# Performance work log

Measured on AMD Instinct MI355X. Metric: run time of the kernel, lower is better.

Reference implementation:

```python
import jax, jax.numpy as jnp
import numpy as np

N = 100000
E = 1600000
BN_EPS = 1e-3  # Keras BatchNormalization default epsilon


def setup_inputs() -> dict:
    key = jax.random.key(0)
    ks = jax.random.split(key, 24)
    inp = {
        'x': jax.random.normal(ks[0], (N, 128), jnp.float32),
        'edge_src': jax.random.randint(ks[1], (E,), 0, N, jnp.int32),
        'edge_dst': jnp.sort(jax.random.randint(ks[2], (E,), 0, N, jnp.int32)),
        'edge_w': jax.random.uniform(ks[3], (E,), jnp.float32),
        'bn1_gamma': jnp.ones((128,), jnp.float32),
        'bn1_beta': jnp.zeros((128,), jnp.float32),
        'bn1_mean': jax.random.normal(ks[4], (128,), jnp.float32),
        'bn1_var': jax.random.uniform(ks[5], (128,), jnp.float32),
        'gat_w': jax.random.normal(ks[6], (128, 128), jnp.float32) * 0.09,
        'gat_a_self': jax.random.normal(ks[7], (128,), jnp.float32) * 0.09,
        'gat_a_nbr': jax.random.normal(ks[8], (128,), jnp.float32) * 0.09,
        'gat_b': jnp.zeros((128,), jnp.float32),
        'bn2_gamma': jnp.ones((128,), jnp.float32),
        'bn2_beta': jnp.zeros((128,), jnp.float32),
        'bn2_mean': jax.random.normal(ks[9], (128,), jnp.float32),
        'bn2_var': jax.random.uniform(ks[10], (128,), jnp.float32),
        'gcn2_w': jax.random.normal(ks[11], (128, 64), jnp.float32) * 0.09,
        'gcn2_b': jnp.zeros((64,), jnp.float32),
        'bn3_gamma': jnp.ones((64,), jnp.float32),
        'bn3_beta': jnp.zeros((64,), jnp.float32),
        'bn3_mean': jax.random.normal(ks[12], (64,), jnp.float32),
        'bn3_var': jax.random.uniform(ks[13], (64,), jnp.float32),
        'gcn3_w': jax.random.normal(ks[14], (64, 32), jnp.float32) * 0.12,
        'gcn3_b': jnp.zeros((32,), jnp.float32),
        'zm_w': jax.random.normal(ks[15], (32, 64), jnp.float32) * 0.18,
        'zm_b': jnp.zeros((64,), jnp.float32),
        'zv_w': jax.random.normal(ks[16], (32, 64), jnp.float32) * 0.18,
        'zv_b': jnp.zeros((64,), jnp.float32),
        'eps': jax.random.normal(ks[17], (N, 64), jnp.float32),
    }
    return inp


def _bn(x, gamma, beta, mean, var):
    # Keras BatchNormalization, inference mode (moving statistics).
    return gamma * (x - mean) * jax.lax.rsqrt(var + BN_EPS) + beta


def _gat(x, edge_src, edge_dst, w, a_self, a_nbr, b, n):
    h = x @ w                                   # [N, C]
    att_i = h @ a_self                          # [N] target score
    att_j = h @ a_nbr                           # [N] source score
    e = jax.nn.leaky_relu(att_i[edge_dst] + att_j[edge_src], 0.2)  # [E]
    m = jax.ops.segment_max(e, edge_dst, num_segments=n)
    p = jnp.exp(e - m[edge_dst])
    s = jax.ops.segment_sum(p, edge_dst, num_segments=n)
    alpha = p / s[edge_dst]                     # segment softmax over in-edges
    out = jax.ops.segment_sum(alpha[:, None] * h[edge_src], edge_dst, num_segments=n)
    return jax.nn.relu(out + b)


def _gcn(x, edge_src, edge_dst, edge_w, w, b, n):
    h = x @ w                                   # [N, C]
    out = jax.ops.segment_sum(edge_w[:, None] * h[edge_src], edge_dst, num_segments=n)
    return jax.nn.relu(out + b)


def reference(x, edge_src, edge_dst, edge_w,
              bn1_gamma, bn1_beta, bn1_mean, bn1_var,
              gat_w, gat_a_self, gat_a_nbr, gat_b,
              bn2_gamma, bn2_beta, bn2_mean, bn2_var,
              gcn2_w, gcn2_b,
              bn3_gamma, bn3_beta, bn3_mean, bn3_var,
              gcn3_w, gcn3_b,
              zm_w, zm_b, zv_w, zv_b, eps):
    n = x.shape[0]
    h = _bn(x, bn1_gamma, bn1_beta, bn1_mean, bn1_var)
    h = _gat(h, edge_src, edge_dst, gat_w, gat_a_self, gat_a_nbr, gat_b, n)
    # dropout layers are identity at inference
    h = _bn(h, bn2_gamma, bn2_beta, bn2_mean, bn2_var)
    h = _gcn(h, edge_src, edge_dst, edge_w, gcn2_w, gcn2_b, n)
    h = _bn(h, bn3_gamma, bn3_beta, bn3_mean, bn3_var)
    h = _gcn(h, edge_src, edge_dst, edge_w, gcn3_w, gcn3_b, n)
    # Flatten on [N, F] is identity
    z_mean = jax.nn.sigmoid(h @ zm_w + zm_b)
    z_log_var = h @ zv_w + zv_b
    z = z_mean + jnp.exp(0.5 * z_log_var) * eps
    return (z_mean, z_log_var, z)
```

## Files before the change

kernel.cpp:

```cpp
#include <hip/hip_runtime.h>
#include <math.h>


#define BN_EPS 1e-3f

__device__ __forceinline__ int swz(int i) { return i + ((i >> 5) << 2); }

__device__ __forceinline__ unsigned bf2(float lo, float hi) {
  unsigned ul = __float_as_uint(lo), uh = __float_as_uint(hi);
  ul = (ul + 0x7FFFu + ((ul >> 16) & 1u)) >> 16;
  uh = (uh + 0x7FFFu + ((uh >> 16) & 1u)) >> 16;
  return ul | (uh << 16);
}

__device__ __forceinline__ float4 ub4(uint2 p) {
  float4 r;
  r.x = __uint_as_float(p.x << 16);
  r.y = __uint_as_float(p.x & 0xFFFF0000u);
  r.z = __uint_as_float(p.y << 16);
  r.w = __uint_as_float(p.y & 0xFFFF0000u);
  return r;
}

__global__ __launch_bounds__(256) void prep_kernel(
    const float* __restrict__ bn1g, const float* __restrict__ bn1b,
    const float* __restrict__ bn1m, const float* __restrict__ bn1v,
    const float* __restrict__ gatw,
    const float* __restrict__ bn2g, const float* __restrict__ bn2b,
    const float* __restrict__ bn2m, const float* __restrict__ bn2v,
    const float* __restrict__ gcn2w,
    const float* __restrict__ bn3g, const float* __restrict__ bn3b,
    const float* __restrict__ bn3m, const float* __restrict__ bn3v,
    const float* __restrict__ gcn3w,
    float* __restrict__ W1f, float* __restrict__ bW1,
    float* __restrict__ W2f, float* __restrict__ bW2,
    float* __restrict__ W3f, float* __restrict__ bW3) {
  __shared__ float a1[128], b1[128], a2[128], b2[128], a3[64], b3[64];
  const int t = threadIdx.x;
  if (t < 128) {
    float a = bn1g[t] * (1.0f / sqrtf(bn1v[t] + BN_EPS));
    a1[t] = a; b1[t] = bn1b[t] - bn1m[t] * a;
    float c = bn2g[t] * (1.0f / sqrtf(bn2v[t] + BN_EPS));
    a2[t] = c; b2[t] = bn2b[t] - bn2m[t] * c;
    if (t < 64) {
      float d = bn3g[t] * (1.0f / sqrtf(bn3v[t] + BN_EPS));
      a3[t] = d; b3[t] = bn3b[t] - bn3m[t] * d;
    }
  }
  __syncthreads();
  for (int idx = t; idx < 128 * 128; idx += 256) W1f[idx] = a1[idx >> 7] * gatw[idx];
  for (int idx = t; idx < 128 * 64; idx += 256)  W2f[idx] = a2[idx >> 6] * gcn2w[idx];
  for (int idx = t; idx < 64 * 32; idx += 256)   W3f[idx] = a3[idx >> 5] * gcn3w[idx];
  if (t < 128) { float s = 0.f; for (int k = 0; k < 128; k++) s += b1[k] * gatw[k * 128 + t]; bW1[t] = s; }
  if (t < 64)  { float s = 0.f; for (int k = 0; k < 128; k++) s += b2[k] * gcn2w[k * 64 + t]; bW2[t] = s; }
  if (t < 32)  { float s = 0.f; for (int k = 0; k < 64; k++)  s += b3[k] * gcn3w[k * 32 + t]; bW3[t] = s; }
}

__global__ __launch_bounds__(256) void rowptr_kernel(
    const int* __restrict__ dst, int* __restrict__ rp, int n, int e) {
  int i = blockIdx.x * 256 + threadIdx.x;
  if (i > n) return;
  int lo = 0, hi = e;
  while (lo < hi) {
    int mid = (lo + hi) >> 1;
    if (dst[mid] < i) lo = mid + 1; else hi = mid;
  }
  rp[i] = lo;
}

template <int K, int C, int NN, int KC, bool DO_ATT>
__global__ __launch_bounds__(256) void gemm_tiled(
    const float* __restrict__ in, const float* __restrict__ Wf,
    const float* __restrict__ bW, unsigned short* __restrict__ outb, int n_nodes,
    const float* __restrict__ aself, const float* __restrict__ anbr,
    float* __restrict__ atti, float* __restrict__ attj) {
  constexpr int NCG = C / 8;
  constexpr int NNG = 256 / NCG;
  constexpr int NT = NNG * NN;
  constexpr int XROW = NT + (NT / 32) * 4;
  constexpr int WROW = C + (C / 32) * 4;
  constexpr int KCV = KC / 4;
  constexpr int CV = C / 4;
  static_assert(!DO_ATT || NCG == 16, "att fusion assumes 16 col-groups");
  __shared__ float xs[KC * XROW];
  __shared__ float wsm[KC * WROW];
  const int node0 = blockIdx.x * NT;
  const float4* __restrict__ x4 = (const float4*)in;
  const int cg = threadIdx.x % NCG;
  const int ng = threadIdx.x / NCG;
  const int xbase = swz(ng * NN);
  const int wbase = swz(cg * 8);
  float acc[NN][8] = {};
#pragma unroll
  for (int kc = 0; kc < K / KC; kc++) {
    if (kc) __syncthreads();
    for (int idx = threadIdx.x; idx < NT * KCV; idx += 256) {
      int row = idx / KCV, kg = idx % KCV;
      int gn = node0 + row;
      if (gn >= n_nodes) gn = n_nodes - 1;
      float4 v = x4[(size_t)gn * (K / 4) + kc * KCV + kg];
      int ns = swz(row);
      xs[(kg * 4 + 0) * XROW + ns] = v.x;
      xs[(kg * 4 + 1) * XROW + ns] = v.y;
      xs[(kg * 4 + 2) * XROW + ns] = v.z;
      xs[(kg * 4 + 3) * XROW + ns] = v.w;
    }
    for (int idx = threadIdx.x; idx < KC * CV; idx += 256) {
      int k = idx / CV, cv = idx % CV;
      float4 v = ((const float4*)Wf)[(size_t)(kc * KC + k) * CV + cv];
      *(float4*)&wsm[k * WROW + swz(cv * 4)] = v;
    }
    __syncthreads();
#pragma unroll 2
    for (int k = 0; k < KC; k++) {
      const float* xr = &xs[k * XROW + xbase];
      const float* wr = &wsm[k * WROW + wbase];
      float4 w0 = *(const float4*)wr;
      float4 w1 = *(const float4*)(wr + 4);
      float4 xa = *(const float4*)xr;
      float xv[NN];
      xv[0] = xa.x; xv[1] = xa.y; xv[2] = xa.z; xv[3] = xa.w;
      if (NN == 8) {
        float4 xb = *(const float4*)(xr + 4);
        xv[4] = xb.x; xv[5] = xb.y; xv[6] = xb.z; xv[7] = xb.w;
      }
#pragma unroll
      for (int i = 0; i < NN; i++) {
        acc[i][0] = fmaf(xv[i], w0.x, acc[i][0]);
        acc[i][1] = fmaf(xv[i], w0.y, acc[i][1]);
        acc[i][2] = fmaf(xv[i], w0.z, acc[i][2]);
        acc[i][3] = fmaf(xv[i], w0.w, acc[i][3]);
        acc[i][4] = fmaf(xv[i], w1.x, acc[i][4]);
        acc[i][5] = fmaf(xv[i], w1.y, acc[i][5]);
        acc[i][6] = fmaf(xv[i], w1.z, acc[i][6]);
        acc[i][7] = fmaf(xv[i], w1.w, acc[i][7]);
      }
    }
  }
  const int c0 = cg * 8;
  const float4 bv0 = *(const float4*)&bW[c0];
  const float4 bv1 = *(const float4*)&bW[c0 + 4];
  float si[NN], sj[NN];
  float4 as0, as1, an0, an1;
  if (DO_ATT) {
    as0 = *(const float4*)&aself[c0]; as1 = *(const float4*)&aself[c0 + 4];
    an0 = *(const float4*)&anbr[c0];  an1 = *(const float4*)&anbr[c0 + 4];
  }
#pragma unroll
  for (int i = 0; i < NN; i++) {
    float4 o0 = {acc[i][0] + bv0.x, acc[i][1] + bv0.y,
                 acc[i][2] + bv0.z, acc[i][3] + bv0.w};
    float4 o1 = {acc[i][4] + bv1.x, acc[i][5] + bv1.y,
                 acc[i][6] + bv1.z, acc[i][7] + bv1.w};
    int gn = node0 + ng * NN + i;
    if (gn < n_nodes) {
      uint4 pk;
      pk.x = bf2(o0.x, o0.y); pk.y = bf2(o0.z, o0.w);
      pk.z = bf2(o1.x, o1.y); pk.w = bf2(o1.z, o1.w);
      *(uint4*)&outb[(size_t)gn * C + c0] = pk;
    }
    if (DO_ATT) {
      si[i] = o0.x * as0.x + o0.y * as0.y + o0.z * as0.z + o0.w * as0.w +
              o1.x * as1.x + o1.y * as1.y + o1.z * as1.z + o1.w * as1.w;
      sj[i] = o0.x * an0.x + o0.y * an0.y + o0.z * an0.z + o0.w * an0.w +
              o1.x * an1.x + o1.y * an1.y + o1.z * an1.z + o1.w * an1.w;
    }
  }
  if (DO_ATT) {
#pragma unroll
    for (int off = 1; off < 16; off <<= 1) {
#pragma unroll
      for (int i = 0; i < NN; i++) {
        si[i] += __shfl_xor(si[i], off);
        sj[i] += __shfl_xor(sj[i], off);
      }
    }
    if (cg == 0) {
#pragma unroll
      for (int i = 0; i < NN; i++) {
        int gn = node0 + ng * NN + i;
        if (gn < n_nodes) { atti[gn] = si[i]; attj[gn] = sj[i]; }
      }
    }
  }
}

__global__ __launch_bounds__(256) void gat_kernel(
    const unsigned short* __restrict__ h1b, const float* __restrict__ att_i,
    const float* __restrict__ att_j, const int* __restrict__ src,
    const int* __restrict__ rp, const float* __restrict__ bias,
    float* __restrict__ out, int n) {
  const int node = (blockIdx.x * 256 + threadIdx.x) >> 6;
  const int lane = threadIdx.x & 63;
  if (node >= n) return;
  const int cg = lane & 31;
  const int eg = lane >> 5;
  const int start = rp[node];
  const int deg = rp[node + 1] - start;
  if (deg == 0) {
    if (eg == 0) {
      float4 b = ((const float4*)bias)[cg];
      float4 o = {fmaxf(b.x, 0.f), fmaxf(b.y, 0.f), fmaxf(b.z, 0.f), fmaxf(b.w, 0.f)};
      ((float4*)out)[(unsigned)node * 32 + cg] = o;
    }
    return;
  }
  const uint2* __restrict__ h2v = (const uint2*)h1b;
  const float ai = att_i[node];
  float4 av[4];
#pragma unroll
  for (int k = 0; k < 4; k++) av[k] = {0.f, 0.f, 0.f, 0.f};
  float ss = 0.f, m_run = -INFINITY;
  for (int chunk = 0; chunk < deg; chunk += 64) {
    const int cnt = min(64, deg - chunk);
    int sv = 0; float v = -INFINITY;
    if (lane < cnt) {
      sv = src[start + chunk + lane];
      float a = ai + att_j[sv];
      v = (a >= 0.f) ? a : 0.2f * a;
    }
    float m = v;
#pragma unroll
    for (int off = 32; off; off >>= 1) m = fmaxf(m, __shfl_xor(m, off));
    const float m_new = fmaxf(m_run, m);
    const float scale = expf(m_run - m_new);
#pragma unroll
    for (int k = 0; k < 4; k++) {
      av[k].x *= scale; av[k].y *= scale; av[k].z *= scale; av[k].w *= scale;
    }
    const float p = (lane < cnt) ? expf(v - m_new) : 0.f;
    float ps = p;
#pragma unroll
    for (int off = 32; off; off >>= 1) ps += __shfl_xor(ps, off);
    ss = ss * scale + ps;
    m_run = m_new;
    for (int j2 = 0; j2 < cnt; j2 += 16) {
      float pk[8]; int sk[8];
#pragma unroll
      for (int k = 0; k < 8; k++) {
        int j = j2 + 2 * k + eg;
        pk[k] = __shfl(p, j);
        sk[k] = __shfl(sv, j);
      }
      uint2 hk[8];
#pragma unroll
      for (int k = 0; k < 8; k++) hk[k] = h2v[(unsigned)sk[k] * 32 + cg];
#pragma unroll
      for (int k = 0; k < 8; k++) {
        float4 hv = ub4(hk[k]);
        av[k & 3].x = fmaf(pk[k], hv.x, av[k & 3].x);
        av[k & 3].y = fmaf(pk[k], hv.y, av[k & 3].y);
        av[k & 3].z = fmaf(pk[k], hv.z, av[k & 3].z);
        av[k & 3].w = fmaf(pk[k], hv.w, av[k & 3].w);
      }
    }
  }
  float4 a0;
  a0.x = av[0].x + av[1].x + av[2].x + av[3].x;
  a0.y = av[0].y + av[1].y + av[2].y + av[3].y;
  a0.z = av[0].z + av[1].z + av[2].z + av[3].z;
  a0.w = av[0].w + av[1].w + av[2].w + av[3].w;
  a0.x += __shfl_xor(a0.x, 32); a0.y += __shfl_xor(a0.y, 32);
  a0.z += __shfl_xor(a0.z, 32); a0.w += __shfl_xor(a0.w, 32);
  if (eg == 0) {
    const float inv = 1.0f / ss;
    float4 b = ((const float4*)bias)[cg];
    float4 o;
    o.x = fmaxf(fmaf(a0.x, inv, b.x), 0.f);
    o.y = fmaxf(fmaf(a0.y, inv, b.y), 0.f);
    o.z = fmaxf(fmaf(a0.z, inv, b.z), 0.f);
    o.w = fmaxf(fmaf(a0.w, inv, b.w), 0.f);
    ((float4*)out)[(unsigned)node * 32 + cg] = o;
  }
}

template <int C, int NCH>
__global__ __launch_bounds__(256) void gcn_agg_kernel(
    const unsigned short* __restrict__ hb, const int* __restrict__ src,
    const float* __restrict__ ew, const int* __restrict__ rp,
    const float* __restrict__ bias, float* __restrict__ out, int n) {
  constexpr int CG = C / 4;
  constexpr int EGN = 64 / CG;
  const int node = (blockIdx.x * 256 + threadIdx.x) >> 6;
  const int lane = threadIdx.x & 63;
  if (node >= n) return;
  const int cg = lane % CG;
  const int eg = lane / CG;
  const int start = rp[node];
  const int deg = rp[node + 1] - start;
  const uint2* __restrict__ h2v = (const uint2*)hb;
  float4 av[4];
#pragma unroll
  for (int k = 0; k < 4; k++) av[k] = {0.f, 0.f, 0.f, 0.f};
  for (int chunk = 0; chunk < deg; chunk += 64) {
    const int cnt = min(64, deg - chunk);
    int sv = 0; float wv = 0.f;
    if (lane < cnt) {
      sv = src[start + chunk + lane];
      wv = ew[start + chunk + lane];
    }
    for (int j2 = 0; j2 < cnt; j2 += NCH * EGN) {
      float wk[NCH]; int sk[NCH];
#pragma unroll
      for (int k = 0; k < NCH; k++) {
        int j = j2 + k * EGN + eg;
        wk[k] = __shfl(wv, j);
        sk[k] = __shfl(sv, j);
      }
      uint2 hk[NCH];
#pragma unroll
      for (int k = 0; k < NCH; k++) hk[k] = h2v[(unsigned)sk[k] * CG + cg];
#pragma unroll
      for (int k = 0; k < NCH; k++) {
        float4 hv = ub4(hk[k]);
        av[k & 3].x = fmaf(wk[k], hv.x, av[k & 3].x);
        av[k & 3].y = fmaf(wk[k], hv.y, av[k & 3].y);
        av[k & 3].z = fmaf(wk[k], hv.z, av[k & 3].z);
        av[k & 3].w = fmaf(wk[k], hv.w, av[k & 3].w);
      }
    }
  }
  float4 a0;
  a0.x = av[0].x + av[1].x + av[2].x + av[3].x;
  a0.y = av[0].y + av[1].y + av[2].y + av[3].y;
  a0.z = av[0].z + av[1].z + av[2].z + av[3].z;
  a0.w = av[0].w + av[1].w + av[2].w + av[3].w;
#pragma unroll
  for (int off = CG; off < 64; off <<= 1) {
    a0.x += __shfl_xor(a0.x, off); a0.y += __shfl_xor(a0.y, off);
    a0.z += __shfl_xor(a0.z, off); a0.w += __shfl_xor(a0.w, off);
  }
  if (eg == 0) {
    float4 b = ((const float4*)bias)[cg];
    float4 o;
    o.x = fmaxf(a0.x + b.x, 0.f); o.y = fmaxf(a0.y + b.y, 0.f);
    o.z = fmaxf(a0.z + b.z, 0.f); o.w = fmaxf(a0.w + b.w, 0.f);
    ((float4*)out)[(unsigned)node * CG + cg] = o;
  }
}

__global__ __launch_bounds__(256) void final_kernel(
    const float* __restrict__ g3, const float* __restrict__ zmw,
    const float* __restrict__ zmb, const float* __restrict__ zvw,
    const float* __restrict__ zvb, const float* __restrict__ eps,
    float* __restrict__ out, int n) {
  __shared__ float wm[32 * 64];
  __shared__ float wv[32 * 64];
  __shared__ float xs[4 * 32];
  for (int idx = threadIdx.x; idx < 2048; idx += 256) {
    wm[idx] = zmw[idx];
    wv[idx] = zvw[idx];
  }
  const float bm = zmb[threadIdx.x & 63];
  const float bv = zvb[threadIdx.x & 63];
  const size_t n64 = (size_t)n * 64;
  for (int pass = 0; pass < 16; pass++) {
    const int nb = blockIdx.x * 64 + pass * 4;
    __syncthreads();
    if (threadIdx.x < 128) {
      size_t idx = (size_t)nb * 32 + threadIdx.x;
      xs[threadIdx.x] = (idx < (size_t)n * 32) ? g3[idx] : 0.f;
    }
    __syncthreads();
    const int node = nb + (threadIdx.x >> 6);
    if (node >= n) continue;
    const int c = threadIdx.x & 63;
    const float* x = &xs[(threadIdx.x >> 6) * 32];
    float am = 0.f, avv = 0.f;
#pragma unroll
    for (int k = 0; k < 32; k++) {
      float xv = x[k];
      am = fmaf(xv, wm[k * 64 + c], am);
      avv = fmaf(xv, wv[k * 64 + c], avv);
    }
    am += bm;
    avv += bv;
    float zm = 1.f / (1.f + expf(-am));
    float ex = expf(fminf(0.5f * avv, 85.0f));
    float z = fmaf(ex, eps[(size_t)node * 64 + c], zm);
    size_t o = (size_t)node * 64 + c;
    out[o] = zm;
    out[n64 + o] = avv;
    out[2 * n64 + o] = z;
  }
}

extern "C" void kernel_launch(void* const* d_in, const int* in_sizes, int n_in,
                              void* d_out, int out_size, void* d_ws, size_t ws_size,
                              hipStream_t stream) {
  const float* x     = (const float*)d_in[0];
  const int*   esrc  = (const int*)d_in[1];
  const int*   edst  = (const int*)d_in[2];
  const float* ew    = (const float*)d_in[3];
  const float* bn1g  = (const float*)d_in[4];
  const float* bn1b  = (const float*)d_in[5];
  const float* bn1m  = (const float*)d_in[6];
  const float* bn1v  = (const float*)d_in[7];
  const float* gatw  = (const float*)d_in[8];
  const float* aself = (const float*)d_in[9];
  const float* anbr  = (const float*)d_in[10];
  const float* gatb  = (const float*)d_in[11];
  const float* bn2g  = (const float*)d_in[12];
  const float* bn2b  = (const float*)d_in[13];
  const float* bn2m  = (const float*)d_in[14];
  const float* bn2v  = (const float*)d_in[15];
  const float* gcn2w = (const float*)d_in[16];
  const float* gcn2b = (const float*)d_in[17];
  const float* bn3g  = (const float*)d_in[18];
  const float* bn3b  = (const float*)d_in[19];
  const float* bn3m  = (const float*)d_in[20];
  const float* bn3v  = (const float*)d_in[21];
  const float* gcn3w = (const float*)d_in[22];
  const float* gcn3b = (const float*)d_in[23];
  const float* zmw   = (const float*)d_in[24];
  const float* zmb   = (const float*)d_in[25];
  const float* zvw   = (const float*)d_in[26];
  const float* zvb   = (const float*)d_in[27];
  const float* eps   = (const float*)d_in[28];
  float* out = (float*)d_out;

  const int n = in_sizes[0] / 128;
  const int E = in_sizes[1];

  char* base = (char*)d_ws;
  size_t off = 0;
  auto alloc = [&](size_t bytes) -> char* {
    char* p = base + off;
    off += (bytes + 255) & ~(size_t)255;
    return p;
  };
  int*   rp   = (int*)alloc((size_t)(n + 1) * 4);
  float* W1f  = (float*)alloc(128 * 128 * 4);
  float* bW1  = (float*)alloc(128 * 4);
  float* W2f  = (float*)alloc(128 * 64 * 4);
  float* bW2  = (float*)alloc(64 * 4);
  float* W3f  = (float*)alloc(64 * 32 * 4);
  float* bW3  = (float*)alloc(32 * 4);
  float* atti = (float*)alloc((size_t)n * 4);
  float* attj = (float*)alloc((size_t)n * 4);
  unsigned short* h1b = (unsigned short*)alloc((size_t)n * 128 * 2);
  float* g1   = (float*)alloc((size_t)n * 128 * 4);
  unsigned short* h2b = (unsigned short*)alloc((size_t)n * 64 * 2);
  float* g2 = (float*)h1b;
  unsigned short* h3b = (unsigned short*)g1;
  float* g3 = (float*)h2b;

  prep_kernel<<<1, 256, 0, stream>>>(bn1g, bn1b, bn1m, bn1v, gatw,
                                     bn2g, bn2b, bn2m, bn2v, gcn2w,
                                     bn3g, bn3b, bn3m, bn3v, gcn3w,
                                     W1f, bW1, W2f, bW2, W3f, bW3);
  rowptr_kernel<<<(n + 256) / 256, 256, 0, stream>>>(edst, rp, n, E);

  gemm_tiled<128, 128, 8, 32, true><<<(n + 127) / 128, 256, 0, stream>>>(
      x, W1f, bW1, h1b, n, aself, anbr, atti, attj);
  gat_kernel<<<(n + 3) / 4, 256, 0, stream>>>(h1b, atti, attj, esrc, rp, gatb, g1, n);

  gemm_tiled<128, 64, 8, 32, false><<<(n + 255) / 256, 256, 0, stream>>>(
      g1, W2f, bW2, h2b, n, nullptr, nullptr, nullptr, nullptr);
  gcn_agg_kernel<64, 8><<<(n + 3) / 4, 256, 0, stream>>>(h2b, esrc, ew, rp, gcn2b, g2, n);

  gemm_tiled<64, 32, 4, 32, false><<<(n + 255) / 256, 256, 0, stream>>>(
      g2, W3f, bW3, h3b, n, nullptr, nullptr, nullptr, nullptr);
  gcn_agg_kernel<32, 4><<<(n + 7) / 8, 256, 0, stream>>>(h3b, esrc, ew, rp, gcn3b, g3, n);

  final_kernel<<<(n + 63) / 64, 256, 0, stream>>>(g3, zmw, zmb, zvw, zvb, eps, out, n);
}
```

Measured before the change: 485.6 us.

## Replace FP32 tiled GEMMs with bf16 MFMA GEMMs using transposed bf16 weights

Swaps the three shared-memory-tiled FP32 FMA GEMMs for a per-wavefront bf16 MFMA (16x16x32) kernel. Each wave handles 16 nodes, converts its input rows to bf16 in registers, and reads transposed bf16 weights produced by the prep kernel straight from global memory, with no LDS staging. The attention dot products are still fused into the epilogue using cross-lane shuffles. This removes FP32 FMA compute and LDS traffic, at the cost of bf16 rounding on inputs and weights and repeated weight reads from global or cache by every wave.

```diff
diff --git a/kernel.cpp b/kernel.cpp
--- a/kernel.cpp
+++ b/kernel.cpp
@@ -4,7 +4,8 @@
 
 #define BN_EPS 1e-3f
 
-__device__ __forceinline__ int swz(int i) { return i + ((i >> 5) << 2); }
+typedef __attribute__((ext_vector_type(8))) short bf16x8;
+typedef __attribute__((ext_vector_type(4))) float f32x4;
 
 __device__ __forceinline__ unsigned bf2(float lo, float hi) {
   unsigned ul = __float_as_uint(lo), uh = __float_as_uint(hi);
@@ -12,7 +13,10 @@
   uh = (uh + 0x7FFFu + ((uh >> 16) & 1u)) >> 16;
   return ul | (uh << 16);
 }
-
+__device__ __forceinline__ unsigned short bf1(float x) {
+  unsigned u = __float_as_uint(x);
+  return (unsigned short)((u + 0x7FFFu + ((u >> 16) & 1u)) >> 16);
+}
 __device__ __forceinline__ float4 ub4(uint2 p) {
   float4 r;
   r.x = __uint_as_float(p.x << 16);
@@ -32,9 +36,9 @@
     const float* __restrict__ bn3g, const float* __restrict__ bn3b,
     const float* __restrict__ bn3m, const float* __restrict__ bn3v,
     const float* __restrict__ gcn3w,
-    float* __restrict__ W1f, float* __restrict__ bW1,
-    float* __restrict__ W2f, float* __restrict__ bW2,
-    float* __restrict__ W3f, float* __restrict__ bW3) {
+    unsigned short* __restrict__ Wt1b, float* __restrict__ bW1,
+    unsigned short* __restrict__ Wt2b, float* __restrict__ bW2,
+    unsigned short* __restrict__ Wt3b, float* __restrict__ bW3) {
   __shared__ float a1[128], b1[128], a2[128], b2[128], a3[64], b3[64];
   const int t = threadIdx.x;
   if (t < 128) {
@@ -48,9 +52,18 @@
     }
   }
   __syncthreads();
-  for (int idx = t; idx < 128 * 128; idx += 256) W1f[idx] = a1[idx >> 7] * gatw[idx];
-  for (int idx = t; idx < 128 * 64; idx += 256)  W2f[idx] = a2[idx >> 6] * gcn2w[idx];
-  for (int idx = t; idx < 64 * 32; idx += 256)   W3f[idx] = a3[idx >> 5] * gcn3w[idx];
+  for (int idx = t; idx < 128 * 128; idx += 256) {
+    int c = idx >> 7, k = idx & 127;
+    Wt1b[idx] = bf1(a1[k] * gatw[k * 128 + c]);
+  }
+  for (int idx = t; idx < 64 * 128; idx += 256) {
+    int c = idx >> 7, k = idx & 127;
+    Wt2b[idx] = bf1(a2[k] * gcn2w[k * 64 + c]);
+  }
+  for (int idx = t; idx < 32 * 64; idx += 256) {
+    int c = idx >> 6, k = idx & 63;
+    Wt3b[idx] = bf1(a3[k] * gcn3w[k * 32 + c]);
+  }
   if (t < 128) { float s = 0.f; for (int k = 0; k < 128; k++) s += b1[k] * gatw[k * 128 + t]; bW1[t] = s; }
   if (t < 64)  { float s = 0.f; for (int k = 0; k < 128; k++) s += b2[k] * gcn2w[k * 64 + t]; bW2[t] = s; }
   if (t < 32)  { float s = 0.f; for (int k = 0; k < 64; k++)  s += b3[k] * gcn3w[k * 32 + t]; bW3[t] = s; }
@@ -68,120 +81,61 @@
   rp[i] = lo;
 }
 
-template <int K, int C, int NN, int KC, bool DO_ATT>
-__global__ __launch_bounds__(256) void gemm_tiled(
-    const float* __restrict__ in, const float* __restrict__ Wf,
-    const float* __restrict__ bW, unsigned short* __restrict__ outb, int n_nodes,
+template <int K, int C, bool DO_ATT>
+__global__ __launch_bounds__(256) void gemm_mfma(
+    const float* __restrict__ in, const unsigned short* __restrict__ Wtb,
+    const float* __restrict__ bW, unsigned short* __restrict__ outb, int n,
     const float* __restrict__ aself, const float* __restrict__ anbr,
     float* __restrict__ atti, float* __restrict__ attj) {
-  constexpr int NCG = C / 8;
-  constexpr int NNG = 256 / NCG;
-  constexpr int NT = NNG * NN;
-  constexpr int XROW = NT + (NT / 32) * 4;
-  constexpr int WROW = C + (C / 32) * 4;
-  constexpr int KCV = KC / 4;
-  constexpr int CV = C / 4;
-  static_assert(!DO_ATT || NCG == 16, "att fusion assumes 16 col-groups");
-  __shared__ float xs[KC * XROW];
-  __shared__ float wsm[KC * WROW];
-  const int node0 = blockIdx.x * NT;
-  const float4* __restrict__ x4 = (const float4*)in;
-  const int cg = threadIdx.x % NCG;
-  const int ng = threadIdx.x / NCG;
-  const int xbase = swz(ng * NN);
-  const int wbase = swz(cg * 8);
-  float acc[NN][8] = {};
-#pragma unroll
-  for (int kc = 0; kc < K / KC; kc++) {
-    if (kc) __syncthreads();
-    for (int idx = threadIdx.x; idx < NT * KCV; idx += 256) {
-      int row = idx / KCV, kg = idx % KCV;
-      int gn = node0 + row;
-      if (gn >= n_nodes) gn = n_nodes - 1;
-      float4 v = x4[(size_t)gn * (K / 4) + kc * KCV + kg];
-      int ns = swz(row);
-      xs[(kg * 4 + 0) * XROW + ns] = v.x;
-      xs[(kg * 4 + 1) * XROW + ns] = v.y;
-      xs[(kg * 4 + 2) * XROW + ns] = v.z;
-      xs[(kg * 4 + 3) * XROW + ns] = v.w;
-    }
-    for (int idx = threadIdx.x; idx < KC * CV; idx += 256) {
-      int k = idx / CV, cv = idx % CV;
-      float4 v = ((const float4*)Wf)[(size_t)(kc * KC + k) * CV + cv];
-      *(float4*)&wsm[k * WROW + swz(cv * 4)] = v;
-    }
-    __syncthreads();
-#pragma unroll 2
-    for (int k = 0; k < KC; k++) {
-      const float* xr = &xs[k * XROW + xbase];
-      const float* wr = &wsm[k * WROW + wbase];
-      float4 w0 = *(const float4*)wr;
-      float4 w1 = *(const float4*)(wr + 4);
-      float4 xa = *(const float4*)xr;
-      float xv[NN];
-      xv[0] = xa.x; xv[1] = xa.y; xv[2] = xa.z; xv[3] = xa.w;
-      if (NN == 8) {
-        float4 xb = *(const float4*)(xr + 4);
-        xv[4] = xb.x; xv[5] = xb.y; xv[6] = xb.z; xv[7] = xb.w;
-      }
-#pragma unroll
-      for (int i = 0; i < NN; i++) {
-        acc[i][0] = fmaf(xv[i], w0.x, acc[i][0]);
-        acc[i][1] = fmaf(xv[i], w0.y, acc[i][1]);
-        acc[i][2] = fmaf(xv[i], w0.z, acc[i][2]);
-        acc[i][3] = fmaf(xv[i], w0.w, acc[i][3]);
-        acc[i][4] = fmaf(xv[i], w1.x, acc[i][4]);
-        acc[i][5] = fmaf(xv[i], w1.y, acc[i][5]);
-        acc[i][6] = fmaf(xv[i], w1.z, acc[i][6]);
-        acc[i][7] = fmaf(xv[i], w1.w, acc[i][7]);
-      }
-    }
-  }
-  const int c0 = cg * 8;
-  const float4 bv0 = *(const float4*)&bW[c0];
-  const float4 bv1 = *(const float4*)&bW[c0 + 4];
-  float si[NN], sj[NN];
-  float4 as0, as1, an0, an1;
-  if (DO_ATT) {
-    as0 = *(const float4*)&aself[c0]; as1 = *(const float4*)&aself[c0 + 4];
-    an0 = *(const float4*)&anbr[c0];  an1 = *(const float4*)&anbr[c0 + 4];
-  }
-#pragma unroll
-  for (int i = 0; i < NN; i++) {
-    float4 o0 = {acc[i][0] + bv0.x, acc[i][1] + bv0.y,
-                 acc[i][2] + bv0.z, acc[i][3] + bv0.w};
-    float4 o1 = {acc[i][4] + bv1.x, acc[i][5] + bv1.y,
-                 acc[i][6] + bv1.z, acc[i][7] + bv1.w};
-    int gn = node0 + ng * NN + i;
-    if (gn < n_nodes) {
-      uint4 pk;
-      pk.x = bf2(o0.x, o0.y); pk.y = bf2(o0.z, o0.w);
-      pk.z = bf2(o1.x, o1.y); pk.w = bf2(o1.z, o1.w);
-      *(uint4*)&outb[(size_t)gn * C + c0] = pk;
-    }
-    if (DO_ATT) {
-      si[i] = o0.x * as0.x + o0.y * as0.y + o0.z * as0.z + o0.w * as0.w +
-              o1.x * as1.x + o1.y * as1.y + o1.z * as1.z + o1.w * as1.w;
-      sj[i] = o0.x * an0.x + o0.y * an0.y + o0.z * an0.z + o0.w * an0.w +
-              o1.x * an1.x + o1.y * an1.y + o1.z * an1.z + o1.w * an1.w;
-    }
-  }
-  if (DO_ATT) {
-#pragma unroll
-    for (int off = 1; off < 16; off <<= 1) {
-#pragma unroll
-      for (int i = 0; i < NN; i++) {
-        si[i] += __shfl_xor(si[i], off);
-        sj[i] += __shfl_xor(sj[i], off);
-      }
-    }
-    if (cg == 0) {
-#pragma unroll
-      for (int i = 0; i < NN; i++) {
-        int gn = node0 + ng * NN + i;
-        if (gn < n_nodes) { atti[gn] = si[i]; attj[gn] = sj[i]; }
-      }
-    }
+  constexpr int KCH = K / 32;
+  constexpr int MB = C / 16;
+  const int wid = (blockIdx.x << 2) + (threadIdx.x >> 6);
+  const int lane = threadIdx.x & 63;
+  const int node0 = wid * 16;
+  if (node0 >= n) return;
+  const int ln = lane & 15;
+  const int kg = lane >> 4;
+  const int nd = node0 + ln;
+  const int ndc = (nd < n) ? nd : (n - 1);
+  bf16x8 bfr[KCH];
+  const float4* __restrict__ inr = (const float4*)(in + (size_t)ndc * K);
+#pragma unroll
+  for (int kc = 0; kc < KCH; kc++) {
+    float4 u0 = inr[kc * 8 + kg * 2];
+    float4 u1 = inr[kc * 8 + kg * 2 + 1];
+    union { uint4 u; bf16x8 v; } pk;
+    pk.u.x = bf2(u0.x, u0.y); pk.u.y = bf2(u0.z, u0.w);
+    pk.u.z = bf2(u1.x, u1.y); pk.u.w = bf2(u1.z, u1.w);
+    bfr[kc] = pk.v;
+  }
+  float sa = 0.f, sj = 0.f;
+#pragma unroll
+  for (int m = 0; m < MB; m++) {
+    f32x4 acc = {0.f, 0.f, 0.f, 0.f};
+#pragma unroll
+    for (int kc = 0; kc < KCH; kc++) {
+      bf16x8 af = *(const bf16x8*)&Wtb[(size_t)(m * 16 + ln) * K + kc * 32 + kg * 8];
+      acc = __builtin_amdgcn_mfma_f32_16x16x32_bf16(af, bfr[kc], acc, 0, 0, 0);
+    }
+    const int c0 = m * 16 + kg * 4;
+    float4 bv = *(const float4*)&bW[c0];
+    float o0 = acc[0] + bv.x, o1 = acc[1] + bv.y;
+    float o2 = acc[2] + bv.z, o3 = acc[3] + bv.w;
+    if (nd < n) {
+      uint2 p; p.x = bf2(o0, o1); p.y = bf2(o2, o3);
+      *(uint2*)&outb[(size_t)nd * C + c0] = p;
+    }
+    if constexpr (DO_ATT) {
+      float4 as = *(const float4*)&aself[c0];
+      float4 an = *(const float4*)&anbr[c0];
+      sa += o0 * as.x + o1 * as.y + o2 * as.z + o3 * as.w;
+      sj += o0 * an.x + o1 * an.y + o2 * an.z + o3 * an.w;
+    }
+  }
+  if constexpr (DO_ATT) {
+    sa += __shfl_xor(sa, 16); sa += __shfl_xor(sa, 32);
+    sj += __shfl_xor(sj, 16); sj += __shfl_xor(sj, 32);
+    if (kg == 0 && nd < n) { atti[nd] = sa; attj[nd] = sj; }
   }
 }
 
@@ -430,11 +384,11 @@
     return p;
   };
   int*   rp   = (int*)alloc((size_t)(n + 1) * 4);
-  float* W1f  = (float*)alloc(128 * 128 * 4);
+  unsigned short* Wt1b = (unsigned short*)alloc(128 * 128 * 2);
   float* bW1  = (float*)alloc(128 * 4);
-  float* W2f  = (float*)alloc(128 * 64 * 4);
+  unsigned short* Wt2b = (unsigned short*)alloc(64 * 128 * 2);
   float* bW2  = (float*)alloc(64 * 4);
-  float* W3f  = (float*)alloc(64 * 32 * 4);
+  unsigned short* Wt3b = (unsigned short*)alloc(32 * 64 * 2);
   float* bW3  = (float*)alloc(32 * 4);
   float* atti = (float*)alloc((size_t)n * 4);
   float* attj = (float*)alloc((size_t)n * 4);
@@ -448,19 +402,22 @@
   prep_kernel<<<1, 256, 0, stream>>>(bn1g, bn1b, bn1m, bn1v, gatw,
                                      bn2g, bn2b, bn2m, bn2v, gcn2w,
                                      bn3g, bn3b, bn3m, bn3v, gcn3w,
-                                     W1f, bW1, W2f, bW2, W3f, bW3);
+                                     Wt1b, bW1, Wt2b, bW2, Wt3b, bW3);
   rowptr_kernel<<<(n + 256) / 256, 256, 0, stream>>>(edst, rp, n, E);
 
-  gemm_tiled<128, 128, 8, 32, true><<<(n + 127) / 128, 256, 0, stream>>>(
-      x, W1f, bW1, h1b, n, aself, anbr, atti, attj);
+  const int gw = (n + 15) / 16;
+  const int gb = (gw + 3) / 4;
+
+  gemm_mfma<128, 128, true><<<gb, 256, 0, stream>>>(
+      x, Wt1b, bW1, h1b, n, aself, anbr, atti, attj);
   gat_kernel<<<(n + 3) / 4, 256, 0, stream>>>(h1b, atti, attj, esrc, rp, gatb, g1, n);
 
-  gemm_tiled<128, 64, 8, 32, false><<<(n + 255) / 256, 256, 0, stream>>>(
-      g1, W2f, bW2, h2b, n, nullptr, nullptr, nullptr, nullptr);
+  gemm_mfma<128, 64, false><<<gb, 256, 0, stream>>>(
+      g1, Wt2b, bW2, h2b, n, nullptr, nullptr, nullptr, nullptr);
   gcn_agg_kernel<64, 8><<<(n + 3) / 4, 256, 0, stream>>>(h2b, esrc, ew, rp, gcn2b, g2, n);
 
-  gemm_tiled<64, 32, 4, 32, false><<<(n + 255) / 256, 256, 0, stream>>>(
-      g2, W3f, bW3, h3b, n, nullptr, nullptr, nullptr, nullptr);
+  gemm_mfma<64, 32, false><<<gb, 256, 0, stream>>>(
+      g2, Wt3b, bW3, h3b, n, nullptr, nullptr, nullptr, nullptr);
   gcn_agg_kernel<32, 4><<<(n + 7) / 8, 256, 0, stream>>>(h3b, esrc, ew, rp, gcn3b, g3, n);
 
   final_kernel<<<(n + 63) / 64, 256, 0, stream>>>(g3, zmw, zmb, zvw, zvb, eps, out, n);
```

Result: faster. 459.7 us (-5.3%).
